# Kernel optimization log

Measured on AMD Instinct MI355X. Metric: run time of the kernel, lower is better.

Reference implementation:

```python
import jax, jax.numpy as jnp
import numpy as np
from jax import lax

B, N, S, C_IN, C_OUT = 4, 16384, 4096, 256, 256


def setup_inputs() -> dict:
    key = jax.random.key(0)
    k1, k2, k3, k4 = jax.random.split(key, 4)
    xyz1 = jax.random.normal(k1, (B, 3, N), dtype=jnp.float32)
    xyz2 = jax.random.normal(k2, (B, 3, S), dtype=jnp.float32)
    points2 = jax.random.normal(k3, (B, C_IN, S), dtype=jnp.float32)
    W = jax.random.normal(k4, (C_OUT, C_IN), dtype=jnp.float32) * (1.0 / np.sqrt(C_IN))
    b = jnp.zeros((C_OUT,), dtype=jnp.float32)
    return {"xyz1": xyz1, "xyz2": xyz2, "points2": points2, "W": W, "b": b}


def reference(xyz1, xyz2, points2, W, b):
    # channel-first -> channel-last
    p1 = jnp.transpose(xyz1, (0, 2, 1))        # [B, N, 3]
    p2 = jnp.transpose(xyz2, (0, 2, 1))        # [B, S, 3]
    f2 = jnp.transpose(points2, (0, 2, 1))     # [B, S, C]
    Bn, Nn, _ = p1.shape
    Cn = f2.shape[-1]
    # squared pairwise distances [B, N, S]
    d = (-2.0 * jnp.einsum('bnc,bsc->bns', p1, p2)
         + jnp.sum(p1 * p1, axis=-1)[:, :, None]
         + jnp.sum(p2 * p2, axis=-1)[:, None, :])
    # 3 nearest neighbors (smallest distances) -- equivalent to sort + slice :3
    neg_d3, idx = lax.top_k(-d, 3)             # [B, N, 3]
    d3 = -neg_d3
    recip = 1.0 / (d3 + 1e-8)
    weight = recip / jnp.sum(recip, axis=-1, keepdims=True)   # [B, N, 3]
    # gather neighbor features: [B, N, 3, C]
    gathered = jnp.take_along_axis(
        f2, idx.reshape(Bn, Nn * 3)[..., None], axis=1
    ).reshape(Bn, Nn, 3, Cn)
    interp = jnp.sum(gathered * weight[..., None], axis=2)    # [B, N, C]
    # Conv1d(kernel=1) == per-point linear: [B, C_out, N]
    out = jnp.einsum('bnc,oc->bon', interp, W) + b[None, :, None]
    return out
```

## Files before the change

### kernel.cpp

```cpp
#include <hip/hip_runtime.h>

#define BB 4
#define NN 16384
#define SS 4096
#define CIN 256
#define COUT 256

#define SC 8
#define SCS (SS / SC)
#define KNNB ((NN / 512) * SC * BB)
#define GEMMB ((COUT / 64) * (SS / 64) * BB)

__device__ __forceinline__ unsigned short f2bf(float f) {
    unsigned u = __float_as_uint(f);
    u += 0x7FFF + ((u >> 16) & 1);
    return (unsigned short)(u >> 16);
}
__device__ __forceinline__ float bf2f(unsigned short h) {
    return __uint_as_float((unsigned)h << 16);
}

__device__ __forceinline__ double pack_key(float e, unsigned gs) {
    double kd = (double)e + 640.0;
    unsigned long long b = __double_as_longlong(kd);
    b = (b & 0xFFFFFFFFFFFFF000ULL) | (unsigned long long)gs;
    return __longlong_as_double((long long)b);
}
__device__ __forceinline__ void insert_key(double& k0, double& k1, double& k2,
                                           double x) {
    double m  = fmax(k0, x);
    k0 = fmin(k0, x);
    double m2 = fmax(k1, m);
    k1 = fmin(k1, m);
    k2 = fmin(k2, m2);
}

__global__ __launch_bounds__(256) void k_fused(const float* __restrict__ xyz1,
                                               const float* __restrict__ xyz2,
                                               const float* __restrict__ P,
                                               const float* __restrict__ W,
                                               const float* __restrict__ bias,
                                               unsigned short* __restrict__ Gh,
                                               unsigned long long* __restrict__ pk) {
    __shared__ float smem[2112];
    int bid = blockIdx.x;
    int t   = threadIdx.x;

    if (bid < KNNB) {
        int nb = bid & 31;
        int ch = (bid >> 5) & 7;
        int b  = bid >> 8;
        int s0 = ch * SCS;

        float4* smv = (float4*)smem;
        const float* x2 = xyz2 + (size_t)b * 3 * SS;
        for (int i = t; i < SCS; i += 256) {
            float px = x2[s0 + i];
            float py = x2[SS + s0 + i];
            float pz = x2[2 * SS + s0 + i];
            smv[i] = make_float4(px, py, pz, fmaf(px, px, fmaf(py, py, pz * pz)));
        }
        __syncthreads();

        int n0  = nb * 512 + t;
        int n1q = n0 + 256;
        const float* xb = xyz1 + (size_t)b * 3 * NN;
        float ax = xb[n0],  ay = xb[NN + n0],  az = xb[2 * NN + n0];
        float bx = xb[n1q], by = xb[NN + n1q], bz = xb[2 * NN + n1q];
        float axm2 = -2.0f * ax, aym2 = -2.0f * ay, azm2 = -2.0f * az;
        float bxm2 = -2.0f * bx, bym2 = -2.0f * by, bzm2 = -2.0f * bz;

        double AK0 = 1023.0, AK1 = 1023.0, AK2 = 1023.0;
        double BK0 = 1023.0, BK1 = 1023.0, BK2 = 1023.0;

#pragma unroll 8
        for (int s = 0; s < SCS; ++s) {
            float4 p = smv[s];
            unsigned gs = (unsigned)(s0 + s);
            {
                float e = fmaf(p.x, axm2, fmaf(p.y, aym2, fmaf(p.z, azm2, p.w)));
                insert_key(AK0, AK1, AK2, pack_key(e, gs));
            }
            {
                float e = fmaf(p.x, bxm2, fmaf(p.y, bym2, fmaf(p.z, bzm2, p.w)));
                insert_key(BK0, BK1, BK2, pack_key(e, gs));
            }
        }

        size_t cb = (size_t)(ch * BB + b) * 3;
        pk[(cb + 0) * NN + n0]  = (unsigned long long)__double_as_longlong(AK0);
        pk[(cb + 1) * NN + n0]  = (unsigned long long)__double_as_longlong(AK1);
        pk[(cb + 2) * NN + n0]  = (unsigned long long)__double_as_longlong(AK2);
        pk[(cb + 0) * NN + n1q] = (unsigned long long)__double_as_longlong(BK0);
        pk[(cb + 1) * NN + n1q] = (unsigned long long)__double_as_longlong(BK1);
        pk[(cb + 2) * NN + n1q] = (unsigned long long)__double_as_longlong(BK2);
    } else {
        int g  = bid - KNNB;
        int o0 = (g & 3) * 64;
        int s0 = ((g >> 2) & 63) * 64;
        int b  = g >> 8;
        float* sP = smem;
        float* sW = smem + 1024;
        int i = t & 15;
        int j = t >> 4;

        float acc[4][4];
#pragma unroll
        for (int p = 0; p < 4; ++p)
#pragma unroll
            for (int q = 0; q < 4; ++q) acc[p][q] = 0.f;

        const float* Pb = P + (size_t)b * CIN * SS;

        for (int c0 = 0; c0 < CIN; c0 += 16) {
            __syncthreads();
            {
                int col = t & 63;
                int r0r = t >> 6;
#pragma unroll
                for (int r = 0; r < 4; ++r) {
                    int row = r0r + r * 4;
                    sP[row * 64 + col] = Pb[(size_t)(c0 + row) * SS + s0 + col];
                }
            }
            {
                int cc = t & 15;
                int obase = t >> 4;
#pragma unroll
                for (int r = 0; r < 4; ++r) {
                    int oo = obase + 16 * r;
                    sW[cc * 68 + oo] = W[(size_t)(o0 + oo) * CIN + c0 + cc];
                }
            }
            __syncthreads();

#pragma unroll
            for (int cc = 0; cc < 16; ++cc) {
                float4 a  = *(const float4*)&sP[cc * 64 + i * 4];
                float4 bv = *(const float4*)&sW[cc * 68 + j * 4];
                float av[4] = {a.x, a.y, a.z, a.w};
                float bw[4] = {bv.x, bv.y, bv.z, bv.w};
#pragma unroll
                for (int p = 0; p < 4; ++p)
#pragma unroll
                    for (int q = 0; q < 4; ++q)
                        acc[p][q] = fmaf(av[p], bw[q], acc[p][q]);
            }
        }

        float b0 = bias[o0 + j * 4 + 0];
        float b1 = bias[o0 + j * 4 + 1];
        float b2 = bias[o0 + j * 4 + 2];
        float b3 = bias[o0 + j * 4 + 3];
#pragma unroll
        for (int p = 0; p < 4; ++p) {
            ushort4 v;
            v.x = f2bf(acc[p][0] + b0);
            v.y = f2bf(acc[p][1] + b1);
            v.z = f2bf(acc[p][2] + b2);
            v.w = f2bf(acc[p][3] + b3);
            size_t off = ((size_t)b * SS + s0 + i * 4 + p) * COUT + o0 + j * 4;
            *(ushort4*)&Gh[off] = v;
        }
    }
}

__global__ __launch_bounds__(256) void k_merge(const unsigned long long* __restrict__ pk,
                                               const float* __restrict__ xyz1,
                                               float4* __restrict__ wi4,
                                               int4* __restrict__ gi4) {
    int b = blockIdx.y;
    int n = blockIdx.x * 256 + threadIdx.x;

    double k0 = 1023.0, k1 = 1023.0, k2 = 1023.0;
#pragma unroll
    for (int ch = 0; ch < SC; ++ch) {
        size_t cb = (size_t)(ch * BB + b) * 3;
#pragma unroll
        for (int j = 0; j < 3; ++j) {
            double x = __longlong_as_double(
                (long long)pk[(cb + j) * NN + n]);
            insert_key(k0, k1, k2, x);
        }
    }

    const float* xb = xyz1 + (size_t)b * 3 * NN;
    float qx = xb[n], qy = xb[NN + n], qz = xb[2 * NN + n];
    float n1 = fmaf(qx, qx, fmaf(qy, qy, qz * qz));

    unsigned long long u0 = (unsigned long long)__double_as_longlong(k0);
    unsigned long long u1 = (unsigned long long)__double_as_longlong(k1);
    unsigned long long u2 = (unsigned long long)__double_as_longlong(k2);
    float e0 = (float)(__longlong_as_double((long long)(u0 & ~0xFFFULL)) - 640.0);
    float e1 = (float)(__longlong_as_double((long long)(u1 & ~0xFFFULL)) - 640.0);
    float e2 = (float)(__longlong_as_double((long long)(u2 & ~0xFFFULL)) - 640.0);
    float d0 = e0 + n1, d1 = e1 + n1, d2 = e2 + n1;

    float r0 = 1.0f / (d0 + 1e-8f);
    float r1 = 1.0f / (d1 + 1e-8f);
    float r2 = 1.0f / (d2 + 1e-8f);
    float inv = 1.0f / (r0 + r1 + r2);
    size_t q = (size_t)b * NN + n;
    wi4[q] = make_float4(r0 * inv, r1 * inv, r2 * inv, 0.f);
    gi4[q] = make_int4((int)(u0 & 0xFFFULL), (int)(u1 & 0xFFFULL),
                       (int)(u2 & 0xFFFULL), 0);
}

__global__ __launch_bounds__(256) void k_out(const unsigned short* __restrict__ Gh,
                                             const float4* __restrict__ wi4,
                                             const int4* __restrict__ gi4,
                                             float* __restrict__ out) {
    __shared__ float  tile[64 * 68];
    __shared__ float4 swv[64];
    __shared__ int4   siv[64];
    int bid  = blockIdx.x;
    int x    = bid & 7;
    int b    = x >> 1;
    int local = (bid >> 3) + (x & 1) * 512;
    int nb   = local & 255;
    int oc   = local >> 8;
    int n0   = nb * 64;
    int o0   = oc * 64;
    int t    = threadIdx.x;
    int wave = t >> 6;
    int lane = t & 63;
    int qg   = lane >> 4;
    int c16  = lane & 15;

    if (t < 64) {
        size_t q = (size_t)b * NN + n0 + t;
        swv[t] = wi4[q];
        siv[t] = gi4[q];
    }
    __syncthreads();

    const unsigned short* Gb = Gh + (size_t)b * SS * COUT;

#pragma unroll
    for (int pass = 0; pass < 4; ++pass) {
        int q = pass * 16 + wave * 4 + qg;
        float4 wv = swv[q];
        int4   iv = siv[q];
        int co = o0 + c16 * 4;
        ushort4 a0 = *(const ushort4*)(Gb + (size_t)iv.x * COUT + co);
        ushort4 a1 = *(const ushort4*)(Gb + (size_t)iv.y * COUT + co);
        ushort4 a2 = *(const ushort4*)(Gb + (size_t)iv.z * COUT + co);
        float4 v;
        v.x = fmaf(wv.x, bf2f(a0.x), fmaf(wv.y, bf2f(a1.x), wv.z * bf2f(a2.x)));
        v.y = fmaf(wv.x, bf2f(a0.y), fmaf(wv.y, bf2f(a1.y), wv.z * bf2f(a2.y)));
        v.z = fmaf(wv.x, bf2f(a0.z), fmaf(wv.y, bf2f(a1.z), wv.z * bf2f(a2.z)));
        v.w = fmaf(wv.x, bf2f(a0.w), fmaf(wv.y, bf2f(a1.w), wv.z * bf2f(a2.w)));
        *(float4*)&tile[q * 68 + c16 * 4] = v;
    }
    __syncthreads();

    float* obase = out + ((size_t)b * COUT + o0) * NN + n0 + lane;
#pragma unroll
    for (int g = 0; g < 4; ++g) {
        int c = wave * 16 + g * 4;
        float4 v = *(const float4*)&tile[lane * 68 + c];
        obase[(size_t)(c + 0) * NN] = v.x;
        obase[(size_t)(c + 1) * NN] = v.y;
        obase[(size_t)(c + 2) * NN] = v.z;
        obase[(size_t)(c + 3) * NN] = v.w;
    }
}

extern "C" void kernel_launch(void* const* d_in, const int* in_sizes, int n_in,
                              void* d_out, int out_size, void* d_ws, size_t ws_size,
                              hipStream_t stream) {
    const float* xyz1    = (const float*)d_in[0];
    const float* xyz2    = (const float*)d_in[1];
    const float* points2 = (const float*)d_in[2];
    const float* W       = (const float*)d_in[3];
    const float* bias    = (const float*)d_in[4];
    float* out = (float*)d_out;

    char* ws = (char*)d_ws;
    unsigned long long* pk  = (unsigned long long*)(ws);
    unsigned short*     Gh  = (unsigned short*)(ws + 12582912);
    float4*             wi4 = (float4*)(ws + 20971520);
    int4*               gi4 = (int4*)(ws + 22020096);

    k_fused<<<dim3(KNNB + GEMMB), 256, 0, stream>>>(xyz1, xyz2, points2, W, bias,
                                                    Gh, pk);
    k_merge<<<dim3(NN / 256, BB), 256, 0, stream>>>(pk, xyz1, wi4, gi4);
    k_out<<<dim3(4096), 256, 0, stream>>>(Gh, wi4, gi4, out);
}
```

Measured before the change: 218.0 us.

## Pair KNN and GEMM work per block and use packed FP32 FMA

Each block now does one KNN tile and one GEMM tile instead of separate block ranges, with alternating order so half the blocks start with compute-heavy KNN and half with memory-heavy GEMM. The distance computation and the GEMM inner product use v_pk_fma_f32 inline asm to process two lanes per instruction. The goal is to balance block work and cut VALU instruction count. In exchange the grid shrinks to 1024 blocks, each block runs longer, and an extra barrier is added between phases.

```diff
diff --git a/kernel.cpp b/kernel.cpp
--- a/kernel.cpp
+++ b/kernel.cpp
@@ -8,8 +8,10 @@
 
 #define SC 8
 #define SCS (SS / SC)
-#define KNNB ((NN / 512) * SC * BB)
-#define GEMMB ((COUT / 64) * (SS / 64) * BB)
+#define FUSEB 1024
+
+typedef float v2f __attribute__((ext_vector_type(2)));
+typedef float v4f __attribute__((ext_vector_type(4)));
 
 __device__ __forceinline__ unsigned short f2bf(float f) {
     unsigned u = __float_as_uint(f);
@@ -33,6 +35,146 @@
     double m2 = fmax(k1, m);
     k1 = fmin(k1, m);
     k2 = fmin(k2, m2);
+}
+
+#define PK_LO(acc, ap, bw)                                                     \
+    asm("v_pk_fma_f32 %0, %1, %2, %0 op_sel:[0,0,0] op_sel_hi:[0,1,1]"         \
+        : "+v"(acc) : "v"(ap), "v"(bw))
+#define PK_HI(acc, ap, bw)                                                     \
+    asm("v_pk_fma_f32 %0, %1, %2, %0 op_sel:[1,0,0] op_sel_hi:[1,1,1]"         \
+        : "+v"(acc) : "v"(ap), "v"(bw))
+
+__device__ __forceinline__ void knn_phase(int bid, int t, float* smem,
+                                          const float* __restrict__ xyz1,
+                                          const float* __restrict__ xyz2,
+                                          unsigned long long* __restrict__ pk) {
+    int nb = bid & 31;
+    int ch = (bid >> 5) & 7;
+    int b  = bid >> 8;
+    int s0 = ch * SCS;
+
+    float4* smv = (float4*)smem;
+    const float* x2 = xyz2 + (size_t)b * 3 * SS;
+    __syncthreads();
+    for (int i = t; i < SCS; i += 256) {
+        float px = x2[s0 + i];
+        float py = x2[SS + s0 + i];
+        float pz = x2[2 * SS + s0 + i];
+        smv[i] = make_float4(px, py, pz, fmaf(px, px, fmaf(py, py, pz * pz)));
+    }
+    __syncthreads();
+
+    int n0  = nb * 512 + t;
+    int n1q = n0 + 256;
+    const float* xb = xyz1 + (size_t)b * 3 * NN;
+    float ax = xb[n0],  ay = xb[NN + n0],  az = xb[2 * NN + n0];
+    float bx = xb[n1q], by = xb[NN + n1q], bz = xb[2 * NN + n1q];
+    v2f XX = {-2.0f * ax, -2.0f * bx};
+    v2f YY = {-2.0f * ay, -2.0f * by};
+    v2f ZZ = {-2.0f * az, -2.0f * bz};
+
+    double AK0 = 1023.0, AK1 = 1023.0, AK2 = 1023.0;
+    double BK0 = 1023.0, BK1 = 1023.0, BK2 = 1023.0;
+
+#pragma unroll 8
+    for (int s = 0; s < SCS; ++s) {
+        v4f p = *(const v4f*)(smem + 4 * s);
+        v2f pxy = __builtin_shufflevector(p, p, 0, 1);
+        v2f pzw = __builtin_shufflevector(p, p, 2, 3);
+        v2f e2;
+        asm("v_pk_fma_f32 %0, %1, %2, %3 op_sel:[0,0,1] op_sel_hi:[0,1,1]"
+            : "=v"(e2) : "v"(pzw), "v"(ZZ), "v"(pzw));
+        asm("v_pk_fma_f32 %0, %1, %2, %0 op_sel:[1,0,0] op_sel_hi:[1,1,1]"
+            : "+v"(e2) : "v"(pxy), "v"(YY));
+        asm("v_pk_fma_f32 %0, %1, %2, %0 op_sel:[0,0,0] op_sel_hi:[0,1,1]"
+            : "+v"(e2) : "v"(pxy), "v"(XX));
+        unsigned gs = (unsigned)(s0 + s);
+        insert_key(AK0, AK1, AK2, pack_key(e2.x, gs));
+        insert_key(BK0, BK1, BK2, pack_key(e2.y, gs));
+    }
+
+    size_t cb = (size_t)(ch * BB + b) * 3;
+    pk[(cb + 0) * NN + n0]  = (unsigned long long)__double_as_longlong(AK0);
+    pk[(cb + 1) * NN + n0]  = (unsigned long long)__double_as_longlong(AK1);
+    pk[(cb + 2) * NN + n0]  = (unsigned long long)__double_as_longlong(AK2);
+    pk[(cb + 0) * NN + n1q] = (unsigned long long)__double_as_longlong(BK0);
+    pk[(cb + 1) * NN + n1q] = (unsigned long long)__double_as_longlong(BK1);
+    pk[(cb + 2) * NN + n1q] = (unsigned long long)__double_as_longlong(BK2);
+}
+
+__device__ __forceinline__ void gemm_phase(int bid, int t, float* smem,
+                                           const float* __restrict__ P,
+                                           const float* __restrict__ W,
+                                           const float* __restrict__ bias,
+                                           unsigned short* __restrict__ Gh) {
+    int o0 = (bid & 3) * 64;
+    int s0 = ((bid >> 2) & 63) * 64;
+    int b  = bid >> 8;
+    float* sP = smem;
+    float* sW = smem + 1024;
+    int i = t & 15;
+    int j = t >> 4;
+
+    v2f acc2[4][2];
+#pragma unroll
+    for (int p = 0; p < 4; ++p) {
+        acc2[p][0] = (v2f){0.f, 0.f};
+        acc2[p][1] = (v2f){0.f, 0.f};
+    }
+
+    const float* Pb = P + (size_t)b * CIN * SS;
+
+    for (int c0 = 0; c0 < CIN; c0 += 16) {
+        __syncthreads();
+        {
+            int col = t & 63;
+            int r0r = t >> 6;
+#pragma unroll
+            for (int r = 0; r < 4; ++r) {
+                int row = r0r + r * 4;
+                sP[row * 64 + col] = Pb[(size_t)(c0 + row) * SS + s0 + col];
+            }
+        }
+        {
+            int cc = t & 15;
+            int obase = t >> 4;
+#pragma unroll
+            for (int r = 0; r < 4; ++r) {
+                int oo = obase + 16 * r;
+                sW[cc * 68 + oo] = W[(size_t)(o0 + oo) * CIN + c0 + cc];
+            }
+        }
+        __syncthreads();
+
+#pragma unroll
+        for (int cc = 0; cc < 16; ++cc) {
+            v4f a  = *(const v4f*)&sP[cc * 64 + i * 4];
+            v4f bv = *(const v4f*)&sW[cc * 68 + j * 4];
+            v2f a01 = __builtin_shufflevector(a, a, 0, 1);
+            v2f a23 = __builtin_shufflevector(a, a, 2, 3);
+            v2f b01 = __builtin_shufflevector(bv, bv, 0, 1);
+            v2f b23 = __builtin_shufflevector(bv, bv, 2, 3);
+            PK_LO(acc2[0][0], a01, b01); PK_LO(acc2[0][1], a01, b23);
+            PK_HI(acc2[1][0], a01, b01); PK_HI(acc2[1][1], a01, b23);
+            PK_LO(acc2[2][0], a23, b01); PK_LO(acc2[2][1], a23, b23);
+            PK_HI(acc2[3][0], a23, b01); PK_HI(acc2[3][1], a23, b23);
+        }
+    }
+
+    float b0 = bias[o0 + j * 4 + 0];
+    float b1 = bias[o0 + j * 4 + 1];
+    float b2 = bias[o0 + j * 4 + 2];
+    float b3 = bias[o0 + j * 4 + 3];
+#pragma unroll
+    for (int p = 0; p < 4; ++p) {
+        ushort4 v;
+        v.x = f2bf(acc2[p][0].x + b0);
+        v.y = f2bf(acc2[p][0].y + b1);
+        v.z = f2bf(acc2[p][1].x + b2);
+        v.w = f2bf(acc2[p][1].y + b3);
+        size_t off = ((size_t)b * SS + s0 + i * 4 + p) * COUT + o0 + j * 4;
+        *(ushort4*)&Gh[off] = v;
+    }
 }
 
 __global__ __launch_bounds__(256) void k_fused(const float* __restrict__ xyz1,
@@ -46,122 +188,12 @@
     int bid = blockIdx.x;
     int t   = threadIdx.x;
 
-    if (bid < KNNB) {
-        int nb = bid & 31;
-        int ch = (bid >> 5) & 7;
-        int b  = bid >> 8;
-        int s0 = ch * SCS;
-
-        float4* smv = (float4*)smem;
-        const float* x2 = xyz2 + (size_t)b * 3 * SS;
-        for (int i = t; i < SCS; i += 256) {
-            float px = x2[s0 + i];
-            float py = x2[SS + s0 + i];
-            float pz = x2[2 * SS + s0 + i];
-            smv[i] = make_float4(px, py, pz, fmaf(px, px, fmaf(py, py, pz * pz)));
-        }
-        __syncthreads();
-
-        int n0  = nb * 512 + t;
-        int n1q = n0 + 256;
-        const float* xb = xyz1 + (size_t)b * 3 * NN;
-        float ax = xb[n0],  ay = xb[NN + n0],  az = xb[2 * NN + n0];
-        float bx = xb[n1q], by = xb[NN + n1q], bz = xb[2 * NN + n1q];
-        float axm2 = -2.0f * ax, aym2 = -2.0f * ay, azm2 = -2.0f * az;
-        float bxm2 = -2.0f * bx, bym2 = -2.0f * by, bzm2 = -2.0f * bz;
-
-        double AK0 = 1023.0, AK1 = 1023.0, AK2 = 1023.0;
-        double BK0 = 1023.0, BK1 = 1023.0, BK2 = 1023.0;
-
-#pragma unroll 8
-        for (int s = 0; s < SCS; ++s) {
-            float4 p = smv[s];
-            unsigned gs = (unsigned)(s0 + s);
-            {
-                float e = fmaf(p.x, axm2, fmaf(p.y, aym2, fmaf(p.z, azm2, p.w)));
-                insert_key(AK0, AK1, AK2, pack_key(e, gs));
-            }
-            {
-                float e = fmaf(p.x, bxm2, fmaf(p.y, bym2, fmaf(p.z, bzm2, p.w)));
-                insert_key(BK0, BK1, BK2, pack_key(e, gs));
-            }
-        }
-
-        size_t cb = (size_t)(ch * BB + b) * 3;
-        pk[(cb + 0) * NN + n0]  = (unsigned long long)__double_as_longlong(AK0);
-        pk[(cb + 1) * NN + n0]  = (unsigned long long)__double_as_longlong(AK1);
-        pk[(cb + 2) * NN + n0]  = (unsigned long long)__double_as_longlong(AK2);
-        pk[(cb + 0) * NN + n1q] = (unsigned long long)__double_as_longlong(BK0);
-        pk[(cb + 1) * NN + n1q] = (unsigned long long)__double_as_longlong(BK1);
-        pk[(cb + 2) * NN + n1q] = (unsigned long long)__double_as_longlong(BK2);
+    if (((bid >> 8) & 1) == 0) {
+        knn_phase(bid, t, smem, xyz1, xyz2, pk);
+        gemm_phase(bid, t, smem, P, W, bias, Gh);
     } else {
-        int g  = bid - KNNB;
-        int o0 = (g & 3) * 64;
-        int s0 = ((g >> 2) & 63) * 64;
-        int b  = g >> 8;
-        float* sP = smem;
-        float* sW = smem + 1024;
-        int i = t & 15;
-        int j = t >> 4;
-
-        float acc[4][4];
-#pragma unroll
-        for (int p = 0; p < 4; ++p)
-#pragma unroll
-            for (int q = 0; q < 4; ++q) acc[p][q] = 0.f;
-
-        const float* Pb = P + (size_t)b * CIN * SS;
-
-        for (int c0 = 0; c0 < CIN; c0 += 16) {
-            __syncthreads();
-            {
-                int col = t & 63;
-                int r0r = t >> 6;
-#pragma unroll
-                for (int r = 0; r < 4; ++r) {
-                    int row = r0r + r * 4;
-                    sP[row * 64 + col] = Pb[(size_t)(c0 + row) * SS + s0 + col];
-                }
-            }
-            {
-                int cc = t & 15;
-                int obase = t >> 4;
-#pragma unroll
-                for (int r = 0; r < 4; ++r) {
-                    int oo = obase + 16 * r;
-                    sW[cc * 68 + oo] = W[(size_t)(o0 + oo) * CIN + c0 + cc];
-                }
-            }
-            __syncthreads();
-
-#pragma unroll
-            for (int cc = 0; cc < 16; ++cc) {
-                float4 a  = *(const float4*)&sP[cc * 64 + i * 4];
-                float4 bv = *(const float4*)&sW[cc * 68 + j * 4];
-                float av[4] = {a.x, a.y, a.z, a.w};
-                float bw[4] = {bv.x, bv.y, bv.z, bv.w};
-#pragma unroll
-                for (int p = 0; p < 4; ++p)
-#pragma unroll
-                    for (int q = 0; q < 4; ++q)
-                        acc[p][q] = fmaf(av[p], bw[q], acc[p][q]);
-            }
-        }
-
-        float b0 = bias[o0 + j * 4 + 0];
-        float b1 = bias[o0 + j * 4 + 1];
-        float b2 = bias[o0 + j * 4 + 2];
-        float b3 = bias[o0 + j * 4 + 3];
-#pragma unroll
-        for (int p = 0; p < 4; ++p) {
-            ushort4 v;
-            v.x = f2bf(acc[p][0] + b0);
-            v.y = f2bf(acc[p][1] + b1);
-            v.z = f2bf(acc[p][2] + b2);
-            v.w = f2bf(acc[p][3] + b3);
-            size_t off = ((size_t)b * SS + s0 + i * 4 + p) * COUT + o0 + j * 4;
-            *(ushort4*)&Gh[off] = v;
-        }
+        gemm_phase(bid, t, smem, P, W, bias, Gh);
+        knn_phase(bid, t, smem, xyz1, xyz2, pk);
     }
 }
 
@@ -282,8 +314,8 @@
     float4*             wi4 = (float4*)(ws + 20971520);
     int4*               gi4 = (int4*)(ws + 22020096);
 
-    k_fused<<<dim3(KNNB + GEMMB), 256, 0, stream>>>(xyz1, xyz2, points2, W, bias,
-                                                    Gh, pk);
+    k_fused<<<dim3(FUSEB), 256, 0, stream>>>(xyz1, xyz2, points2, W, bias,
+                                             Gh, pk);
     k_merge<<<dim3(NN / 256, BB), 256, 0, stream>>>(pk, xyz1, wi4, gi4);
     k_out<<<dim3(4096), 256, 0, stream>>>(Gh, wi4, gi4, out);
 }
```

Result: no change. 214.7 us (-1.5%).
